# Performance work log

Hardware: AMD Instinct MI355X
Metric: run time of the kernel (lower is better)

Reference implementation:

```python
import jax, jax.numpy as jnp
import numpy as np

EPS = 1e-8
TOP_K = 3  # hardcoded in the original forward (torch.topk(sims, 3))


def setup_inputs() -> dict:
    key = jax.random.key(0)
    ks = jax.random.split(key, 6)
    n1, d1 = 4096, 1024
    n2, d2 = 4096, 4096
    V = jax.random.normal(ks[0], (n1, d1), dtype=jnp.float32)
    X = jax.random.normal(ks[1], (n2, d2), dtype=jnp.float32)
    # nn.Linear(visual_dim, text_dim): weight [d2, d1], bias [d2]
    Wv = jax.random.normal(ks[2], (d2, d1), dtype=jnp.float32) * (1.0 / np.sqrt(d1))
    bv = jax.random.normal(ks[3], (d2,), dtype=jnp.float32) * 0.01
    # nn.Linear(top_k, 1): weight [1, 3], bias [1]
    Wf = jax.random.normal(ks[4], (1, TOP_K), dtype=jnp.float32) * (1.0 / np.sqrt(TOP_K))
    bf = jax.random.normal(ks[5], (1,), dtype=jnp.float32) * 0.01
    return {"V": V, "X": X, "Wv": Wv, "bv": bv, "Wf": Wf, "bf": bf}


def reference(V, X, Wv, bv, Wf, bf):
    # project visual tokens into text space: [n1, d2]
    V_proj = V @ Wv.T + bv
    # cosine similarity: normalize queries (full-vector norm) and keys (row norm)
    Qn = X / (jnp.linalg.norm(X, axis=1, keepdims=True) + EPS)          # [n2, d2]
    Kn = V_proj / (jnp.linalg.norm(V_proj, axis=1, keepdims=True) + EPS)  # [n1, d2]
    sims = Qn @ Kn.T                                                     # [n2, n1]
    # per-text-token top-k visual tokens
    _, topk_idx = jax.lax.top_k(sims, TOP_K)                             # [n2, k]
    gathered = V_proj[topk_idx]                                          # [n2, k, d2]
    # fuse over k: Linear(k -> 1) applied along the top-k axis, squeeze -> [n2, d2]
    V_aligned = jnp.einsum('nkd,k->nd', gathered, Wf[0]) + bf[0]
    return jnp.concatenate([V_aligned, X], axis=0)                       # [2*n2, d2]
```

## Files before the change

### kernel.cpp

```cpp
#include <hip/hip_runtime.h>
#include <hip/hip_bf16.h>

constexpr int N1 = 4096;
constexpr int D1 = 1024;
constexpr int N2 = 4096;
constexpr int D2 = 4096;

#define FNEG  (-3.402823466e+38f)
#define IDX_INF 0x7FFFFFFF
#define NCHUNK 32
#define CPR (NCHUNK * 6)
#define FCAP 1024
#define ZCH 8
#define ZB 32
#define CERT_TH 2.0e-4f

using s16x8 = __attribute__((ext_vector_type(8))) short;
using f32x4 = __attribute__((ext_vector_type(4))) float;

static __device__ __forceinline__ unsigned short f2bf(float x) {
    unsigned int u = __float_as_uint(x);
    unsigned int r = (u + 0x7FFFu + ((u >> 16) & 1u)) >> 16;
    return (unsigned short)r;
}
static __device__ __forceinline__ float bf2f(unsigned short v) {
    return __uint_as_float((unsigned)v << 16);
}
static __device__ __forceinline__ void splitbf(float x, unsigned short& h,
                                               unsigned short& l) {
    unsigned short hh = f2bf(x);
    float r = x - __uint_as_float((unsigned)hh << 16);
    h = hh; l = f2bf(r);
}
static __device__ __forceinline__ int swz(int row, int g) {
    return row * 32 + ((g ^ (row & 3)) << 3);
}

static __device__ __forceinline__ void stageF32(const float* src, int ld,
    int rowbase, int k0, unsigned short* H, unsigned short* L, int tid)
{
    const int r = tid >> 1, half = tid & 1;
    const float* p = src + (size_t)(rowbase + r) * ld + k0 + half * 16;
#pragma unroll
    for (int gg = 0; gg < 2; ++gg) {
        const int g = half * 2 + gg;
        float4 v0 = *(const float4*)(p + gg * 8);
        float4 v1 = *(const float4*)(p + gg * 8 + 4);
        float xs[8] = {v0.x, v0.y, v0.z, v0.w, v1.x, v1.y, v1.z, v1.w};
        s16x8 hv, lv;
#pragma unroll
        for (int e = 0; e < 8; ++e) {
            unsigned short h, l; splitbf(xs[e], h, l);
            hv[e] = (short)h; lv[e] = (short)l;
        }
        const int a = swz(r, g);
        *(s16x8*)&H[a] = hv;
        *(s16x8*)&L[a] = lv;
    }
}

static __device__ __forceinline__ void gl_lds16(const void* g, void* l)
{
    __builtin_amdgcn_global_load_lds(
        (const __attribute__((address_space(1))) void*)g,
        (__attribute__((address_space(3))) void*)l, 16, 0, 0);
}

static __device__ __forceinline__ void stageSplitGL(const unsigned short* Hs,
    const unsigned short* Ls, int ld, int rowbase, int k0,
    unsigned short* H, unsigned short* L, int lane, int w)
{
#pragma unroll
    for (int t = 0; t < 2; ++t) {
        const int chunk = w * 128 + t * 64 + lane;
        const int row = chunk >> 2;
        const int gp  = chunk & 3;
        const int g   = gp ^ (row & 3);
        const unsigned short* sh =
            Hs + (size_t)(rowbase + row) * ld + k0 + g * 8;
        const unsigned short* sl =
            Ls + (size_t)(rowbase + row) * ld + k0 + g * 8;
        unsigned short* dh = H + (size_t)(w * 128 + t * 64) * 8;
        unsigned short* dl = L + (size_t)(w * 128 + t * 64) * 8;
        gl_lds16(sh, dh);
        gl_lds16(sl, dl);
    }
}

static __device__ __forceinline__ void stageWvTpre(const unsigned short* Wh,
    const unsigned short* Wl, int k0, int tn,
    unsigned short* H, unsigned short* L, int tid)
{
    const int kk = tid >> 3, cg = tid & 7;
    const int g = kk >> 3, idx = kk & 7;
    const unsigned short* ph = Wh + (size_t)(k0 + kk) * D1 + tn + cg * 16;
    const unsigned short* pl = Wl + (size_t)(k0 + kk) * D1 + tn + cg * 16;
#pragma unroll
    for (int q = 0; q < 4; ++q) {
        ushort4 vh = *(const ushort4*)(ph + q * 4);
        ushort4 vl = *(const ushort4*)(pl + q * 4);
        unsigned short hs[4] = {vh.x, vh.y, vh.z, vh.w};
        unsigned short ls[4] = {vl.x, vl.y, vl.z, vl.w};
#pragma unroll
        for (int e = 0; e < 4; ++e) {
            const int cc = cg * 16 + q * 4 + e;
            const int a = cc * 32 + ((g ^ (cc & 3)) << 3) + idx;
            H[a] = hs[e]; L[a] = ls[e];
        }
    }
}

static __device__ __forceinline__ s16x8 fragRead(const unsigned short* B,
                                                 int rowbase, int lane)
{
    const int row = rowbase + (lane & 15);
    const int g = lane >> 4;
    return *(const s16x8*)&B[row * 32 + ((g ^ (row & 3)) << 3)];
}

#define MFMA3(ACC, AH, AL, BH, BL)                                          \
    ACC = __builtin_amdgcn_mfma_f32_16x16x32_bf16(AH, BH, ACC, 0, 0, 0);    \
    ACC = __builtin_amdgcn_mfma_f32_16x16x32_bf16(AH, BL, ACC, 0, 0, 0);    \
    ACC = __builtin_amdgcn_mfma_f32_16x16x32_bf16(AL, BH, ACC, 0, 0, 0);

static __device__ __forceinline__ void top6f(float v, int i, float* vv, int* ii)
{
#pragma unroll
    for (int s = 0; s < 6; ++s) {
        if (v > vv[s]) {
#pragma unroll
            for (int t = 5; t > s; --t) { vv[t] = vv[t-1]; ii[t] = ii[t-1]; }
            vv[s] = v; ii[s] = i;
            break;
        }
    }
}

__global__ __launch_bounds__(256)
void kDetect(const float* c1, const float* c2, int* flags, int* flagCnt)
{
    __shared__ float red[256];
    float d = 0.f;
    for (int i = threadIdx.x; i < 4096; i += 256) {
        float a = c1[i], b = c2[i];
        d += a * a - b * b;
    }
    red[threadIdx.x] = d;
    __syncthreads();
    for (int st = 128; st > 0; st >>= 1) {
        if (threadIdx.x < st) red[threadIdx.x] += red[threadIdx.x + st];
        __syncthreads();
    }
    if (threadIdx.x == 0) {
        flags[0] = (red[0] < 0.f) ? 1 : 0;
        flagCnt[0] = 0;
    }
}

__global__ __launch_bounds__(256)
void kSplit(const float* src, unsigned short* h, unsigned short* l, int n4)
{
    int i = blockIdx.x * 256 + threadIdx.x;
    if (i >= n4) return;
    float4 v = *(const float4*)(src + (size_t)i * 4);
    float xs[4] = {v.x, v.y, v.z, v.w};
    ushort4 hv, lv;
    unsigned short hh, ll;
    splitbf(xs[0], hh, ll); hv.x = hh; lv.x = ll;
    splitbf(xs[1], hh, ll); hv.y = hh; lv.y = ll;
    splitbf(xs[2], hh, ll); hv.z = hh; lv.z = ll;
    splitbf(xs[3], hh, ll); hv.w = hh; lv.w = ll;
    *(ushort4*)(h + (size_t)i * 4) = hv;
    *(ushort4*)(l + (size_t)i * 4) = lv;
}

__global__ __launch_bounds__(256)
void kSvec(const float* X, const float* bv, float* sXF, double* sXD)
{
    __shared__ double red[256];
    const int row = blockIdx.x;
    double s = 0.0;
    for (int n = threadIdx.x; n < D2; n += 256)
        s += (double)X[(size_t)row * D2 + n] * (double)bv[n];
    red[threadIdx.x] = s;
    __syncthreads();
    for (int st = 128; st > 0; st >>= 1) {
        if (threadIdx.x < st) red[threadIdx.x] += red[threadIdx.x + st];
        __syncthreads();
    }
    if (threadIdx.x == 0) { sXF[row] = (float)red[0]; sXD[row] = red[0]; }
}

__global__ __launch_bounds__(256)
void kNormMfma(const unsigned short* c1h, const unsigned short* c1l,
               const unsigned short* c2h, const unsigned short* c2l,
               const float* bv, const int* flags, float* partial,
               unsigned short* Vph)
{
    const unsigned short* Vh  = flags[0] ? c2h : c1h;
    const unsigned short* Vl  = flags[0] ? c2l : c1l;
    const unsigned short* Wvh = flags[0] ? c1h : c2h;
    const unsigned short* Wvl = flags[0] ? c1l : c2l;
    __shared__ __align__(16) char pool[65536];
    __shared__ float partH[128][2];
    const int tid = threadIdx.x;
    const int lane = tid & 63, w = tid >> 6;
    const int wr = w >> 1, wc = w & 1;
    const int tm = blockIdx.y * 128;
    const int tn = blockIdx.x * 128;

    f32x4 acc[4][4];
#pragma unroll
    for (int i = 0; i < 4; ++i)
#pragma unroll
        for (int j = 0; j < 4; ++j) acc[i][j] = (f32x4){0.f, 0.f, 0.f, 0.f};

    {
        unsigned short* B0 = (unsigned short*)pool;
        stageSplitGL(Vh,  Vl,  D1, tm, 0, B0,        B0 + 4096,  lane, w);
        stageSplitGL(Wvh, Wvl, D1, tn, 0, B0 + 8192, B0 + 12288, lane, w);
    }
    __syncthreads();

    for (int k0 = 0; k0 < D1; k0 += 32) {
        const int cur = (k0 >> 5) & 1;
        unsigned short* CB = (unsigned short*)(pool + cur * 32768);
        if (k0 + 32 < D1) {
            unsigned short* NB = (unsigned short*)(pool + (cur ^ 1) * 32768);
            stageSplitGL(Vh,  Vl,  D1, tm, k0 + 32, NB,        NB + 4096,
                         lane, w);
            stageSplitGL(Wvh, Wvl, D1, tn, k0 + 32, NB + 8192, NB + 12288,
                         lane, w);
        }
        s16x8 ah[4], al[4], bh[4], bl[4];
#pragma unroll
        for (int f = 0; f < 4; ++f) {
            ah[f] = fragRead(CB,         wr * 64 + f * 16, lane);
            al[f] = fragRead(CB + 4096,  wr * 64 + f * 16, lane);
            bh[f] = fragRead(CB + 8192,  wc * 64 + f * 16, lane);
            bl[f] = fragRead(CB + 12288, wc * 64 + f * 16, lane);
        }
#pragma unroll
        for (int fm = 0; fm < 4; ++fm)
#pragma unroll
            for (int fn = 0; fn < 4; ++fn) {
                MFMA3(acc[fm][fn], ah[fm], al[fm], bh[fn], bl[fn]);
            }
        __syncthreads();
    }

    float bvv[4];
#pragma unroll
    for (int fn = 0; fn < 4; ++fn)
        bvv[fn] = bv[tn + wc * 64 + fn * 16 + (lane & 15)];
#pragma unroll
    for (int fm = 0; fm < 4; ++fm)
#pragma unroll
        for (int r = 0; r < 4; ++r) {
            const int lrow = wr * 64 + fm * 16 + (lane >> 4) * 4 + r;
            float rs = 0.f;
#pragma unroll
            for (int fn = 0; fn < 4; ++fn) {
                float v = acc[fm][fn][r] + bvv[fn];
                Vph[(size_t)(tm + lrow) * D2 +
                    (tn + wc * 64 + fn * 16 + (lane & 15))] = f2bf(v);
                rs += v * v;
            }
            rs += __shfl_xor(rs, 1, 64);
            rs += __shfl_xor(rs, 2, 64);
            rs += __shfl_xor(rs, 4, 64);
            rs += __shfl_xor(rs, 8, 64);
            if ((lane & 15) == 0) partH[lrow][wc] = rs;
        }
    __syncthreads();
    if (tid < 128)
        partial[(size_t)(tm + tid) * 32 + blockIdx.x] =
            partH[tid][0] + partH[tid][1];
}

__global__ __launch_bounds__(256)
void kInv(const float* partial, float* invnF, double* invnD)
{
    int j = blockIdx.x * 256 + threadIdx.x;
    double s = 0.0;
    for (int cb = 0; cb < 32; ++cb) s += (double)partial[(size_t)j * 32 + cb];
    double iv = 1.0 / (sqrt(s) + 1e-8);
    invnD[j] = iv;
    invnF[j] = (float)iv;
}

__global__ __launch_bounds__(256)
void mfmaZ(const float* X,
           const unsigned short* c1h, const unsigned short* c1l,
           const unsigned short* c2h, const unsigned short* c2l,
           const int* flags, unsigned short* Zh, unsigned short* Zl)
{
    const unsigned short* Wvh = flags[0] ? c1h : c2h;
    const unsigned short* Wvl = flags[0] ? c1l : c2l;
    __shared__ unsigned short AH[4096], AL[4096], BH[4096], BL[4096];
    const int tid = threadIdx.x;
    const int lane = tid & 63, w = tid >> 6;
    const int wr = w >> 1, wc = w & 1;
    const int tm = blockIdx.y * 128;
    const int tn = blockIdx.x * 128;

    f32x4 acc[4][4];
#pragma unroll
    for (int i = 0; i < 4; ++i)
#pragma unroll
        for (int j = 0; j < 4; ++j) acc[i][j] = (f32x4){0.f, 0.f, 0.f, 0.f};

    for (int k0 = 0; k0 < D2; k0 += 32) {
        stageF32(X, D2, tm, k0, AH, AL, tid);
        stageWvTpre(Wvh, Wvl, k0, tn, BH, BL, tid);
        __syncthreads();
        s16x8 ah[4], al[4], bh[4], bl[4];
#pragma unroll
        for (int f = 0; f < 4; ++f) {
            ah[f] = fragRead(AH, wr * 64 + f * 16, lane);
            al[f] = fragRead(AL, wr * 64 + f * 16, lane);
            bh[f] = fragRead(BH, wc * 64 + f * 16, lane);
            bl[f] = fragRead(BL, wc * 64 + f * 16, lane);
        }
#pragma unroll
        for (int fm = 0; fm < 4; ++fm)
#pragma unroll
            for (int fn = 0; fn < 4; ++fn) {
                MFMA3(acc[fm][fn], ah[fm], al[fm], bh[fn], bl[fn]);
            }
        __syncthreads();
    }
#pragma unroll
    for (int fm = 0; fm < 4; ++fm)
#pragma unroll
        for (int fn = 0; fn < 4; ++fn)
#pragma unroll
            for (int r = 0; r < 4; ++r) {
                int row = tm + wr * 64 + fm * 16 + (lane >> 4) * 4 + r;
                int col = tn + wc * 64 + fn * 16 + (lane & 15);
                unsigned short h, l;
                splitbf(acc[fm][fn][r], h, l);
                size_t o = (size_t)row * D1 + col;
                Zh[o] = h; Zl[o] = l;
            }
}

__global__ __launch_bounds__(256)
void mfmaS(const unsigned short* Zh, const unsigned short* Zl,
           const unsigned short* c1h, const unsigned short* c1l,
           const unsigned short* c2h, const unsigned short* c2l,
           const float* invnF, const float* sXF, const int* flags,
           float* candV, int* candI)
{
    const unsigned short* Vh = flags[0] ? c2h : c1h;
    const unsigned short* Vl = flags[0] ? c2l : c1l;
    __shared__ __align__(16) char pool[65536];
    float* Ct   = (float*)pool;
    float* pv   = (float*)(pool + 33792);
    int*   pi   = (int*)  (pool + 36864);
    float* invs = (float*)(pool + 39936);

    const int tid = threadIdx.x;
    const int lane = tid & 63, w = tid >> 6;
    const int wr = w >> 1, wc = w & 1;
    const int tm = blockIdx.y * 128;
    const int tn = blockIdx.x * 128;

    f32x4 acc[4][4];
#pragma unroll
    for (int i = 0; i < 4; ++i)
#pragma unroll
        for (int j = 0; j < 4; ++j) acc[i][j] = (f32x4){0.f, 0.f, 0.f, 0.f};

    {
        unsigned short* B0 = (unsigned short*)pool;
        stageSplitGL(Zh, Zl, D1, tm, 0, B0,        B0 + 4096,  lane, w);
        stageSplitGL(Vh, Vl, D1, tn, 0, B0 + 8192, B0 + 12288, lane, w);
    }
    __syncthreads();

    for (int k0 = 0; k0 < D1; k0 += 32) {
        const int cur = (k0 >> 5) & 1;
        unsigned short* CB = (unsigned short*)(pool + cur * 32768);
        if (k0 + 32 < D1) {
            unsigned short* NB = (unsigned short*)(pool + (cur ^ 1) * 32768);
            stageSplitGL(Zh, Zl, D1, tm, k0 + 32, NB,        NB + 4096,
                         lane, w);
            stageSplitGL(Vh, Vl, D1, tn, k0 + 32, NB + 8192, NB + 12288,
                         lane, w);
        }
        s16x8 ah[4], al[4], bh[4], bl[4];
#pragma unroll
        for (int f = 0; f < 4; ++f) {
            ah[f] = fragRead(CB,         wr * 64 + f * 16, lane);
            al[f] = fragRead(CB + 4096,  wr * 64 + f * 16, lane);
            bh[f] = fragRead(CB + 8192,  wc * 64 + f * 16, lane);
            bl[f] = fragRead(CB + 12288, wc * 64 + f * 16, lane);
        }
#pragma unroll
        for (int fm = 0; fm < 4; ++fm)
#pragma unroll
            for (int fn = 0; fn < 4; ++fn) {
                MFMA3(acc[fm][fn], ah[fm], al[fm], bh[fn], bl[fn]);
            }
        __syncthreads();
    }

    if (tid < 128) invs[tid] = invnF[tn + tid];
    for (int h = 0; h < 2; ++h) {
        __syncthreads();
        if (wr == h) {
#pragma unroll
            for (int fm = 0; fm < 4; ++fm)
#pragma unroll
                for (int fn = 0; fn < 4; ++fn)
#pragma unroll
                    for (int r = 0; r < 4; ++r) {
                        int lr = fm * 16 + (lane >> 4) * 4 + r;
                        int c  = wc * 64 + fn * 16 + (lane & 15);
                        Ct[lr * 132 + c] = acc[fm][fn][r];
                    }
        }
        __syncthreads();
        if (tid < 128) {
            int r = tid >> 1, seg = tid & 1;
            float sxf = sXF[tm + h * 64 + r];
            float vv[6]; int ii[6];
#pragma unroll
            for (int s = 0; s < 6; ++s) { vv[s] = FNEG; ii[s] = IDX_INF; }
            for (int cc = 0; cc < 64; ++cc) {
                int c = seg * 64 + cc;
                float v = (Ct[r * 132 + c] + sxf) * invs[c];
                top6f(v, tn + c, vv, ii);
            }
#pragma unroll
            for (int s = 0; s < 6; ++s) {
                pv[(r * 2 + seg) * 6 + s] = vv[s];
                pi[(r * 2 + seg) * 6 + s] = ii[s];
            }
        }
        __syncthreads();
        if (tid < 64) {
            float vv[6]; int ii[6];
#pragma unroll
            for (int s = 0; s < 6; ++s) { vv[s] = FNEG; ii[s] = IDX_INF; }
            for (int seg = 0; seg < 2; ++seg)
                for (int s = 0; s < 6; ++s)
                    top6f(pv[(tid * 2 + seg) * 6 + s],
                          pi[(tid * 2 + seg) * 6 + s], vv, ii);
            int row = tm + h * 64 + tid;
#pragma unroll
            for (int s = 0; s < 6; ++s) {
                candV[(size_t)row * CPR + blockIdx.x * 6 + s] = vv[s];
                candI[(size_t)row * CPR + blockIdx.x * 6 + s] = ii[s];
            }
        }
    }
}

__global__ __launch_bounds__(64)
void kMergeCert(const float* candV, const int* candI, int* tidx,
                int* flagCnt, int* flagRow, int* flagCand)
{
    if (threadIdx.x != 0) return;
    const int row = blockIdx.x;
    float vv[6]; int ii[6];
    for (int s = 0; s < 6; ++s) { vv[s] = FNEG; ii[s] = IDX_INF; }
    for (int c = 0; c < CPR; ++c)
        top6f(candV[(size_t)row * CPR + c], candI[(size_t)row * CPR + c],
              vv, ii);
    tidx[row * 3 + 0] = ii[0];
    tidx[row * 3 + 1] = ii[1];
    tidx[row * 3 + 2] = ii[2];
    bool cert = (vv[0] - vv[1] > CERT_TH) &&
                (vv[1] - vv[2] > CERT_TH) &&
                (vv[2] - vv[3] > CERT_TH);
    if (!cert) {
        int idx = atomicAdd(flagCnt, 1);
        if (idx < FCAP) {
            flagRow[idx] = row;
            for (int s = 0; s < 6; ++s) flagCand[idx * 6 + s] = ii[s];
        }
    }
}

__global__ __launch_bounds__(128)
void kZx(const int* flagCnt, const int* flagRow,
         const float* c1, const float* c2, const int* flags,
         const float* X, double* Zx)
{
    const float* Wv = flags[0] ? c1 : c2;
    const int nact = min(flagCnt[0], FCAP);
    const int cc = blockIdx.x;
    const int zb = blockIdx.y;
    const int tid = threadIdx.x;
    const int c = cc * 128 + tid;
    __shared__ float Xs[ZCH][1024];
    __shared__ int   rows[ZCH];

    for (int z0 = zb * ZCH; z0 < nact; z0 += ZB * ZCH) {
        const int na = min(ZCH, nact - z0);
        __syncthreads();
        if (tid < ZCH)
            rows[tid] = flagRow[z0 + min(tid, na - 1)];
        __syncthreads();

        double acc[ZCH];
#pragma unroll
        for (int zz = 0; zz < ZCH; ++zz) acc[zz] = 0.0;

        for (int n0 = 0; n0 < D2; n0 += 1024) {
            __syncthreads();
            for (int idx = tid * 4; idx < ZCH * 1024; idx += 128 * 4) {
                const int zz = idx >> 10, i = idx & 1023;
                *(float4*)&Xs[zz][i] =
                    *(const float4*)(X + (size_t)rows[zz] * D2 + n0 + i);
            }
            __syncthreads();
#pragma unroll 4
            for (int i = 0; i < 1024; ++i) {
                const double wvd = (double)Wv[(size_t)(n0 + i) * D1 + c];
#pragma unroll
                for (int zz = 0; zz < ZCH; ++zz)
                    acc[zz] = fma((double)Xs[zz][i], wvd, acc[zz]);
            }
        }
#pragma unroll
        for (int zz = 0; zz < ZCH; ++zz)
            if (zz < na)
                Zx[(size_t)(z0 + zz) * D1 + c] = acc[zz];
    }
}

__global__ __launch_bounds__(64)
void kScore6(const int* flagCnt, const int* flagRow, const int* flagCand,
             const double* Zx, const float* c1, const float* c2,
             const int* flags, const double* sXD, const double* invnD,
             int* tidx)
{
    const int z = blockIdx.x;
    if (z >= flagCnt[0] || z >= FCAP) return;
    const float* V = flags[0] ? c2 : c1;
    const int lane = threadIdx.x;

    double zr[16];
#pragma unroll
    for (int t = 0; t < 16; ++t)
        zr[t] = Zx[(size_t)z * D1 + t * 64 + lane];

    double sc[6]; int js[6];
    for (int s = 0; s < 6; ++s) {
        js[s] = flagCand[z * 6 + s];
        const float* vr = V + (size_t)js[s] * D1;
        double d = 0.0;
#pragma unroll
        for (int t = 0; t < 16; ++t)
            d = fma(zr[t], (double)vr[t * 64 + lane], d);
#pragma unroll
        for (int off = 1; off < 64; off <<= 1)
            d += __shfl_xor(d, off, 64);
        sc[s] = d;
    }
    if (lane == 0) {
        const int row = flagRow[z];
        const double sx = sXD[row];
        for (int s = 0; s < 6; ++s)
            sc[s] = (sc[s] + sx) * invnD[js[s]];
        int ord[6] = {0, 1, 2, 3, 4, 5};
        for (int a = 0; a < 5; ++a)
            for (int b = a + 1; b < 6; ++b) {
                bool swp = (sc[ord[b]] > sc[ord[a]]) ||
                           (sc[ord[b]] == sc[ord[a]] &&
                            js[ord[b]] < js[ord[a]]);
                if (swp) { int t = ord[a]; ord[a] = ord[b]; ord[b] = t; }
            }
        tidx[row * 3 + 0] = js[ord[0]];
        tidx[row * 3 + 1] = js[ord[1]];
        tidx[row * 3 + 2] = js[ord[2]];
    }
}

__global__ __launch_bounds__(256)
void kGatherVa(const unsigned short* Vph, const int* tidx,
               const float* Wf, const float* bfp, float* outVa)
{
    const int row = blockIdx.x;
    const int i0 = tidx[row*3+0], i1 = tidx[row*3+1], i2 = tidx[row*3+2];
    const float w0 = Wf[0], w1 = Wf[1], w2 = Wf[2], b = bfp[0];
    const unsigned short* p0 = Vph + (size_t)i0 * D2;
    const unsigned short* p1 = Vph + (size_t)i1 * D2;
    const unsigned short* p2 = Vph + (size_t)i2 * D2;
    float* o = outVa + (size_t)row * D2;
    for (int c = threadIdx.x * 8; c < D2; c += 256 * 8) {
        s16x8 a = *(const s16x8*)(p0 + c);
        s16x8 d = *(const s16x8*)(p1 + c);
        s16x8 e = *(const s16x8*)(p2 + c);
        float out[8];
#pragma unroll
        for (int t = 0; t < 8; ++t)
            out[t] = w0 * bf2f((unsigned short)a[t]) +
                     w1 * bf2f((unsigned short)d[t]) +
                     w2 * bf2f((unsigned short)e[t]) + b;
        *(float4*)(o + c)     = *(float4*)&out[0];
        *(float4*)(o + c + 4) = *(float4*)&out[4];
    }
}

extern "C" void kernel_launch(void* const* d_in, const int* in_sizes, int n_in,
                              void* d_out, int out_size, void* d_ws, size_t ws_size,
                              hipStream_t stream)
{
    const float *c1 = nullptr, *c2 = nullptr, *X = nullptr;
    const float *bv = nullptr, *Wf = nullptr, *bfp = nullptr;
    for (int i = 0; i < n_in; ++i) {
        const float* p = (const float*)d_in[i];
        switch (in_sizes[i]) {
            case 16777216: X = p; break;
            case 4194304:  if (!c1) c1 = p; else c2 = p; break;
            case 4096:     bv = p; break;
            case 3:        Wf = p; break;
            case 1:        bfp = p; break;
            default: break;
        }
    }

    float* out_f = (float*)d_out;
    float* outVa = out_f;
    float* outX  = out_f + (size_t)N2 * D2;

    int* flags   = (int*)d_ws;
    int* flagCnt = (int*)((char*)d_ws + 128);
    char* C0 = (char*)d_ws + 1024;
    float*  sXF     = (float*) (C0);
    float*  invnF   = (float*) (C0 + 16384);
    int*    tidx    = (int*)   (C0 + 32768);
    double* sXD     = (double*)(C0 + 81920);
    double* invnD   = (double*)(C0 + 114688);
    float*  partial = (float*) (C0 + 147456);
    float*  candV   = (float*) (C0 + 671744);
    int*    candI   = (int*)   (C0 + 3817472);
    int*    flagRow = (int*)   (C0 + 6963200);
    int*    flagCand= (int*)   (C0 + 6967296);
    unsigned short* Zh = (unsigned short*)(C0 + 8388608);
    unsigned short* Zl = (unsigned short*)(C0 + 16777216);

    char* up = (char*)outX;
    unsigned short* c1h = (unsigned short*)(up);
    unsigned short* c1l = (unsigned short*)(up + 8388608);
    unsigned short* c2h = (unsigned short*)(up + 16777216);
    unsigned short* c2l = (unsigned short*)(up + 25165824);
    unsigned short* Vph = (unsigned short*)(up + 33554432);
    double* Zx = (double*)(up);

    kDetect<<<1, 256, 0, stream>>>(c1, c2, flags, flagCnt);
    kSplit<<<4096, 256, 0, stream>>>(c1, c1h, c1l, N1 * D1 / 4);
    kSplit<<<4096, 256, 0, stream>>>(c2, c2h, c2l, N1 * D1 / 4);
    kSvec<<<N2, 256, 0, stream>>>(X, bv, sXF, sXD);

    dim3 gN(D2 / 128, N1 / 128);
    kNormMfma<<<gN, 256, 0, stream>>>(c1h, c1l, c2h, c2l, bv, flags,
                                      partial, Vph);
    kInv<<<16, 256, 0, stream>>>(partial, invnF, invnD);

    dim3 gZ(D1 / 128, N2 / 128);
    mfmaZ<<<gZ, 256, 0, stream>>>(X, c1h, c1l, c2h, c2l, flags, Zh, Zl);

    dim3 gS(N1 / 128, N2 / 128);
    mfmaS<<<gS, 256, 0, stream>>>(Zh, Zl, c1h, c1l, c2h, c2l,
                                  invnF, sXF, flags, candV, candI);

    kMergeCert<<<N2, 64, 0, stream>>>(candV, candI, tidx,
                                      flagCnt, flagRow, flagCand);

    dim3 gX(8, ZB);
    kZx<<<gX, 128, 0, stream>>>(flagCnt, flagRow, c1, c2, flags, X, Zx);
    kScore6<<<FCAP, 64, 0, stream>>>(flagCnt, flagRow, flagCand, Zx,
                                     c1, c2, flags, sXD, invnD, tidx);

    kGatherVa<<<N2, 256, 0, stream>>>(Vph, tidx, Wf, bfp, outVa);

    hipMemcpyAsync(outX, X, (size_t)N2 * D2 * sizeof(float),
                   hipMemcpyDeviceToDevice, stream);
}
```

Before: 1.503 ms.

## Pre-split X to bf16 hi/lo and double-buffer mfmaZ LDS staging

X is split into bf16 high/low halves once by a new kSplit launch into scratch space in the output buffer, so mfmaZ no longer converts fp32 to split bf16 inside its k-loop for every tile. mfmaZ now loads X tiles with direct global-to-LDS copies and uses a two-stage LDS ping-pong buffer, prefetching the next k-slice while the MFMAs run on the current one. This removes the per-tile conversion work and hides load latency, at the cost of an extra full pass over X (64MB read, 64MB written) and doubled LDS use, which may lower occupancy.

```diff
diff --git a/kernel.cpp b/kernel.cpp
--- a/kernel.cpp
+++ b/kernel.cpp
@@ -34,29 +34,6 @@
 }
 static __device__ __forceinline__ int swz(int row, int g) {
     return row * 32 + ((g ^ (row & 3)) << 3);
-}
-
-static __device__ __forceinline__ void stageF32(const float* src, int ld,
-    int rowbase, int k0, unsigned short* H, unsigned short* L, int tid)
-{
-    const int r = tid >> 1, half = tid & 1;
-    const float* p = src + (size_t)(rowbase + r) * ld + k0 + half * 16;
-#pragma unroll
-    for (int gg = 0; gg < 2; ++gg) {
-        const int g = half * 2 + gg;
-        float4 v0 = *(const float4*)(p + gg * 8);
-        float4 v1 = *(const float4*)(p + gg * 8 + 4);
-        float xs[8] = {v0.x, v0.y, v0.z, v0.w, v1.x, v1.y, v1.z, v1.w};
-        s16x8 hv, lv;
-#pragma unroll
-        for (int e = 0; e < 8; ++e) {
-            unsigned short h, l; splitbf(xs[e], h, l);
-            hv[e] = (short)h; lv[e] = (short)l;
-        }
-        const int a = swz(r, g);
-        *(s16x8*)&H[a] = hv;
-        *(s16x8*)&L[a] = lv;
-    }
 }
 
 static __device__ __forceinline__ void gl_lds16(const void* g, void* l)
@@ -290,14 +267,14 @@
 }
 
 __global__ __launch_bounds__(256)
-void mfmaZ(const float* X,
+void mfmaZ(const unsigned short* Xh, const unsigned short* Xl,
            const unsigned short* c1h, const unsigned short* c1l,
            const unsigned short* c2h, const unsigned short* c2l,
            const int* flags, unsigned short* Zh, unsigned short* Zl)
 {
     const unsigned short* Wvh = flags[0] ? c1h : c2h;
     const unsigned short* Wvl = flags[0] ? c1l : c2l;
-    __shared__ unsigned short AH[4096], AL[4096], BH[4096], BL[4096];
+    __shared__ __align__(16) char pool[65536];
     const int tid = threadIdx.x;
     const int lane = tid & 63, w = tid >> 6;
     const int wr = w >> 1, wc = w & 1;
@@ -310,17 +287,28 @@
 #pragma unroll
         for (int j = 0; j < 4; ++j) acc[i][j] = (f32x4){0.f, 0.f, 0.f, 0.f};
 
+    {
+        unsigned short* B0 = (unsigned short*)pool;
+        stageSplitGL(Xh, Xl, D2, tm, 0, B0, B0 + 4096, lane, w);
+        stageWvTpre(Wvh, Wvl, 0, tn, B0 + 8192, B0 + 12288, tid);
+    }
+    __syncthreads();
+
     for (int k0 = 0; k0 < D2; k0 += 32) {
-        stageF32(X, D2, tm, k0, AH, AL, tid);
-        stageWvTpre(Wvh, Wvl, k0, tn, BH, BL, tid);
-        __syncthreads();
+        const int cur = (k0 >> 5) & 1;
+        unsigned short* CB = (unsigned short*)(pool + cur * 32768);
+        if (k0 + 32 < D2) {
+            unsigned short* NB = (unsigned short*)(pool + (cur ^ 1) * 32768);
+            stageSplitGL(Xh, Xl, D2, tm, k0 + 32, NB, NB + 4096, lane, w);
+            stageWvTpre(Wvh, Wvl, k0 + 32, tn, NB + 8192, NB + 12288, tid);
+        }
         s16x8 ah[4], al[4], bh[4], bl[4];
 #pragma unroll
         for (int f = 0; f < 4; ++f) {
-            ah[f] = fragRead(AH, wr * 64 + f * 16, lane);
-            al[f] = fragRead(AL, wr * 64 + f * 16, lane);
-            bh[f] = fragRead(BH, wc * 64 + f * 16, lane);
-            bl[f] = fragRead(BL, wc * 64 + f * 16, lane);
+            ah[f] = fragRead(CB,         wr * 64 + f * 16, lane);
+            al[f] = fragRead(CB + 4096,  wr * 64 + f * 16, lane);
+            bh[f] = fragRead(CB + 8192,  wc * 64 + f * 16, lane);
+            bl[f] = fragRead(CB + 12288, wc * 64 + f * 16, lane);
         }
 #pragma unroll
         for (int fm = 0; fm < 4; ++fm)
@@ -652,9 +640,13 @@
     unsigned short* Vph = (unsigned short*)(up + 33554432);
     double* Zx = (double*)(up);
 
+    unsigned short* Xh = (unsigned short*)d_out;
+    unsigned short* Xl = (unsigned short*)((char*)d_out + 33554432);
+
     kDetect<<<1, 256, 0, stream>>>(c1, c2, flags, flagCnt);
     kSplit<<<4096, 256, 0, stream>>>(c1, c1h, c1l, N1 * D1 / 4);
     kSplit<<<4096, 256, 0, stream>>>(c2, c2h, c2l, N1 * D1 / 4);
+    kSplit<<<16384, 256, 0, stream>>>(X, Xh, Xl, N2 * D2 / 4);
     kSvec<<<N2, 256, 0, stream>>>(X, bv, sXF, sXD);
 
     dim3 gN(D2 / 128, N1 / 128);
@@ -663,7 +655,7 @@
     kInv<<<16, 256, 0, stream>>>(partial, invnF, invnD);
 
     dim3 gZ(D1 / 128, N2 / 128);
-    mfmaZ<<<gZ, 256, 0, stream>>>(X, c1h, c1l, c2h, c2l, flags, Zh, Zl);
+    mfmaZ<<<gZ, 256, 0, stream>>>(Xh, Xl, c1h, c1l, c2h, c2l, flags, Zh, Zl);
 
     dim3 gS(N1 / 128, N2 / 128);
     mfmaS<<<gS, 256, 0, stream>>>(Zh, Zl, c1h, c1l, c2h, c2l,
```

After: 1.524 ms. No clear change (+1.4%).
